# Optimization experiments

Hardware: AMD Instinct MI355X
Metric: run time of the kernel (lower is better)

The kernel has to match this reference:

```python
import jax, jax.numpy as jnp
import numpy as np

EPS = 1e-12

def l2_normalize(x, axis=-1):
    # matches torch F.normalize(p=2, dim=1, eps=1e-12) for 2D input
    n = jnp.sqrt(jnp.sum(x * x, axis=axis, keepdims=True))
    return x / jnp.maximum(n, EPS)

def setup_inputs() -> dict:
    key = jax.random.key(0)
    ks = jax.random.split(key, 7)
    N, D = 8192, 256
    s = 1.0 / np.sqrt(D)
    x = jax.random.normal(ks[0], (N, D), dtype=jnp.float32)
    Wq = jax.random.uniform(ks[1], (D, D), jnp.float32, -s, s)
    bq = jax.random.uniform(ks[2], (D,), jnp.float32, -s, s)
    Wk = jax.random.uniform(ks[3], (D, D), jnp.float32, -s, s)
    bk = jax.random.uniform(ks[4], (D,), jnp.float32, -s, s)
    Wv = jax.random.uniform(ks[5], (D, D), jnp.float32, -s, s)
    bv = jax.random.uniform(ks[6], (D,), jnp.float32, -s, s)
    return {"x": x, "Wq": Wq, "bq": bq, "Wk": Wk, "bk": bk, "Wv": Wv, "bv": bv}

def reference(x, Wq, bq, Wk, bk, Wv, bv):
    q = l2_normalize(x @ Wq.T + bq)           # [N, D]
    k = l2_normalize(x @ Wk.T + bk)           # [N, D]
    v = x @ Wv.T + bv                         # [N, D]
    cos_sim = q @ k.T                         # [N, N]
    w = jax.nn.relu(cos_sim)
    # zero diagonal, then renormalize rows to sum 1
    N = w.shape[0]
    w = jnp.where(jnp.eye(N, dtype=bool), 0.0, w)
    w = w / jnp.maximum(jnp.sum(w, axis=-1, keepdims=True), EPS)
    return w @ v + x
```

## Files before the change

### kernel.cpp

```cpp
#include <hip/hip_runtime.h>

#define NROWS 8192
#define DDIM  256
#define KSPLIT 4
#define BM 128
#define BK 64
#define NT (NROWS / KSPLIT / BK)

typedef __bf16 bf16x8 __attribute__((ext_vector_type(8)));
typedef float  f32x4  __attribute__((ext_vector_type(4)));
typedef float  f32x16 __attribute__((ext_vector_type(16)));

typedef __attribute__((address_space(1))) unsigned int uint_gas;
typedef __attribute__((address_space(3))) unsigned int uint_las;

__device__ __forceinline__ void gload_lds16(const void* g, void* l) {
  __builtin_amdgcn_global_load_lds((const uint_gas*)g, (uint_las*)l, 16, 0, 0);
}

__device__ __forceinline__ unsigned int f2bf_bits(float f) {
  union { float f; unsigned int u; } v; v.f = f;
  unsigned int r = v.u + 0x7FFFu + ((v.u >> 16) & 1u);
  return r >> 16;
}
__device__ __forceinline__ float bf2f(unsigned int b) {
  union { unsigned int u; float f; } v; v.u = b << 16;
  return v.f;
}
__device__ __forceinline__ unsigned int pack2bf(float a, float b) {
  union { unsigned int u; __bf16 h[2]; } p;
  p.h[0] = (__bf16)a; p.h[1] = (__bf16)b;
  return p.u;
}
__device__ __forceinline__ unsigned short f2h_bits(float f) {
  union { _Float16 h; unsigned short u; } c; c.h = (_Float16)f;
  return c.u;
}
__device__ __forceinline__ float h2f(unsigned short u) {
  union { unsigned short u; _Float16 h; } c; c.u = u;
  return (float)c.h;
}
__device__ __forceinline__ bf16x8 cvt8(const float* p) {
  float4 f0 = *(const float4*)p;
  float4 f1 = *(const float4*)(p + 4);
  union { bf16x8 v; unsigned short s[8]; } u;
  u.s[0] = (unsigned short)f2bf_bits(f0.x);
  u.s[1] = (unsigned short)f2bf_bits(f0.y);
  u.s[2] = (unsigned short)f2bf_bits(f0.z);
  u.s[3] = (unsigned short)f2bf_bits(f0.w);
  u.s[4] = (unsigned short)f2bf_bits(f1.x);
  u.s[5] = (unsigned short)f2bf_bits(f1.y);
  u.s[6] = (unsigned short)f2bf_bits(f1.z);
  u.s[7] = (unsigned short)f2bf_bits(f1.w);
  return u.v;
}

#define NWFRAG (3 * 16 * 8 * 64)
__global__ __launch_bounds__(256) void convert_kernel(
    const float* __restrict__ wq, const float* __restrict__ wk,
    const float* __restrict__ wv, unsigned short* __restrict__ Wp)
{
  int fid = blockIdx.x * 256 + threadIdx.x;
  if (fid >= NWFRAG) return;
  int l = fid & 63, ks = (fid >> 6) & 7, ct = (fid >> 9) & 15, out = fid >> 13;
  const float* src = (out == 0) ? wq : (out == 1) ? wk : wv;
  unsigned short* dst = Wp + (size_t)fid * 8;
  int row = ct * 16 + (l & 15), col = ks * 32 + (l >> 4) * 8;
  const float* p = src + (size_t)row * DDIM + col;
  float4 f0 = *(const float4*)p;
  float4 f1 = *(const float4*)(p + 4);
  ushort4 o0, o1;
  o0.x = (unsigned short)f2bf_bits(f0.x); o0.y = (unsigned short)f2bf_bits(f0.y);
  o0.z = (unsigned short)f2bf_bits(f0.z); o0.w = (unsigned short)f2bf_bits(f0.w);
  o1.x = (unsigned short)f2bf_bits(f1.x); o1.y = (unsigned short)f2bf_bits(f1.y);
  o1.z = (unsigned short)f2bf_bits(f1.z); o1.w = (unsigned short)f2bf_bits(f1.w);
  *(ushort4*)dst = o0;
  *(ushort4*)(dst + 4) = o1;
}

__global__ __launch_bounds__(256) void qkv_kernel(
    const float* __restrict__ bq, const float* __restrict__ bk, const float* __restrict__ bv,
    const float* __restrict__ x, const unsigned short* __restrict__ Wp,
    unsigned short* __restrict__ qb, unsigned short* __restrict__ kb,
    unsigned short* __restrict__ vtp)
{
  __shared__ unsigned short vstage[DDIM * 72];
  const int t = threadIdx.x;
  const int w = t >> 6, l = t & 63;
  const int c = l & 15, g = l >> 4;
  const int out = blockIdx.x / 128;
  const int mb  = blockIdx.x % 128;
  const int row0 = mb * 64;
  const int rw = row0 + w * 16;

  bf16x8 a[8];
  #pragma unroll
  for (int ks = 0; ks < 8; ks++)
    a[ks] = cvt8(x + (size_t)(rw + c) * DDIM + ks * 32 + g * 8);

  const float* bias = (out == 0) ? bq : (out == 1) ? bk : bv;
  f32x4 vals[16];
  #pragma unroll
  for (int ct = 0; ct < 16; ct++) {
    f32x4 acc = {0.f, 0.f, 0.f, 0.f};
    #pragma unroll
    for (int ks = 0; ks < 8; ks++) {
      bf16x8 b = *(const bf16x8*)(Wp + ((size_t)((out * 16 + ct) * 8 + ks) * 64 + l) * 8);
      acc = __builtin_amdgcn_mfma_f32_16x16x32_bf16(a[ks], b, acc, 0, 0, 0);
    }
    float bias_v = bias[ct * 16 + c];
    #pragma unroll
    for (int r = 0; r < 4; r++) acc[r] += bias_v;
    vals[ct] = acc;
  }
  if (out < 2) {
    #pragma unroll
    for (int r = 0; r < 4; r++) {
      float ss = 0.f;
      #pragma unroll
      for (int ct = 0; ct < 16; ct++) ss += vals[ct][r] * vals[ct][r];
      ss += __shfl_xor(ss, 1); ss += __shfl_xor(ss, 2);
      ss += __shfl_xor(ss, 4); ss += __shfl_xor(ss, 8);
      float inv = 1.f / fmaxf(sqrtf(ss), 1e-12f);
      #pragma unroll
      for (int ct = 0; ct < 16; ct++) vals[ct][r] *= inv;
    }
    unsigned short* dst = (out == 0) ? qb : kb;
    #pragma unroll
    for (int ct = 0; ct < 16; ct++) {
      #pragma unroll
      for (int r = 0; r < 4; r++) {
        unsigned int bits = f2bf_bits(vals[ct][r]);
        unsigned int ob = (unsigned int)__shfl_xor((int)bits, 1);
        if (!(l & 1))
          *(unsigned int*)(dst + (size_t)(rw + g * 4 + r) * DDIM + ct * 16 + c) =
              bits | (ob << 16);
      }
    }
  } else {
    #pragma unroll
    for (int ct = 0; ct < 16; ct++)
      #pragma unroll
      for (int r = 0; r < 4; r++)
        vstage[(ct * 16 + c) * 72 + (w * 16 + g * 4 + r)] =
            (unsigned short)f2bf_bits(vals[ct][r]);
    __syncthreads();
    unsigned short* wdst = vtp + (size_t)mb * 16384;
    #pragma unroll
    for (int p = 0; p < 8; p++) {
      int n = p * 256 + t;
      int dg = ((n >> 8) << 5) + (n & 31);
      int s  = (n >> 5) & 7;
      *(uint4*)(wdst + (size_t)n * 8) = *(const uint4*)(vstage + dg * 72 + s * 8);
    }
  }
}

__global__ __launch_bounds__(1024, 4) void attn_kernel(
    const unsigned short* __restrict__ qb, const unsigned short* __restrict__ kb,
    const unsigned short* __restrict__ vtp,
    unsigned short* __restrict__ nump, float* __restrict__ denp)
{
  __shared__ __align__(16) char smem[98304];
  char* kbuf = smem;
  char* Pb   = smem + 65536;

  const int t = threadIdx.x;
  const int w = t >> 6, l = t & 63;
  const int l31 = l & 31, hi = l >> 5;
  const int rw = w & 7;
  const int ts = t & 511;
  const int bid = blockIdx.x;
  const int split = bid & (KSPLIT - 1);
  const int mb = bid >> 2;
  const int q0 = mb * BM;
  const int kbase0 = split * (NROWS / KSPLIT);
  const char* kbc = (const char*)kb;
  const char* vtc = (const char*)vtp;

  if (w < 8) {
    const int sr = rw >> 1, sc = rw & 1;
    const int qrow = sr * 32 + l31;
    const int qrowg = q0 + qrow;
    const int krl = sc * 32 + l31;

    bf16x8 qa[16];
    {
      const unsigned short* qrowp = qb + (size_t)(q0 + qrow) * DDIM + hi * 8;
      #pragma unroll
      for (int m = 0; m < 16; m++) qa[m] = *(const bf16x8*)(qrowp + m * 16);
    }
    float denl = 0.f;

    auto stageK = [&](int buf, int it) {
      const char* ksrc = kbc + (size_t)(kbase0 + it * BK) * 512;
      #pragma unroll
      for (int i = 0; i < 4; i++) {
        int n = i * 512 + ts;
        int row = n >> 5, slot = n & 31;
        gload_lds16(ksrc + row * 512 + (((slot - row) & 31) << 4),
                    kbuf + buf * 32768 + i * 8192 + rw * 1024);
      }
    };

    stageK(0, 0);
    asm volatile("s_waitcnt vmcnt(0)" ::: "memory");
    __builtin_amdgcn_sched_barrier(0);
    __builtin_amdgcn_s_barrier();
    __builtin_amdgcn_sched_barrier(0);

    for (int it = 0; it < NT; ++it) {
      const int cur = it & 1;
      if (it + 1 < NT) stageK(cur ^ 1, it + 1);
      __builtin_amdgcn_sched_barrier(0);

      const char* kcur = kbuf + cur * 32768;
      f32x16 sacc = (f32x16){0.f};
      #pragma unroll
      for (int m = 0; m < 16; m++) {
        bf16x8 kf = *(const bf16x8*)(kcur + krl * 512 +
                                     (((m * 2 + hi + krl) & 31) << 4));
        sacc = __builtin_amdgcn_mfma_f32_32x32x16_bf16(kf, qa[m], sacc, 0, 0, 0);
      }
      char* pbase = Pb + cur * 16384 + sr * 4096 + l31 * 16 + hi * 8;
      const int kbase = kbase0 + it * BK;
      if (__builtin_expect(kbase < q0 + BM && q0 < kbase + BK, 0)) {
        const int dref = qrowg - (kbase + sc * 32 + hi * 4);
        #pragma unroll
        for (int q = 0; q < 4; q++) {
          float v0 = fmaxf(sacc[4 * q + 0], 0.f);
          float v1 = fmaxf(sacc[4 * q + 1], 0.f);
          float v2 = fmaxf(sacc[4 * q + 2], 0.f);
          float v3 = fmaxf(sacc[4 * q + 3], 0.f);
          const int d = dref - 8 * q;
          v0 = (d == 0) ? 0.f : v0;
          v1 = (d == 1) ? 0.f : v1;
          v2 = (d == 2) ? 0.f : v2;
          v3 = (d == 3) ? 0.f : v3;
          denl += (v0 + v1) + (v2 + v3);
          uint2 d2;
          d2.x = pack2bf(v0, v1);
          d2.y = pack2bf(v2, v3);
          *(uint2*)(pbase + (sc * 4 + q) * 512) = d2;
        }
      } else {
        #pragma unroll
        for (int q = 0; q < 4; q++) {
          float v0 = fmaxf(sacc[4 * q + 0], 0.f);
          float v1 = fmaxf(sacc[4 * q + 1], 0.f);
          float v2 = fmaxf(sacc[4 * q + 2], 0.f);
          float v3 = fmaxf(sacc[4 * q + 3], 0.f);
          denl += (v0 + v1) + (v2 + v3);
          uint2 d2;
          d2.x = pack2bf(v0, v1);
          d2.y = pack2bf(v2, v3);
          *(uint2*)(pbase + (sc * 4 + q) * 512) = d2;
        }
      }
      asm volatile("s_waitcnt vmcnt(0) lgkmcnt(0)" ::: "memory");
      __builtin_amdgcn_sched_barrier(0);
      __builtin_amdgcn_s_barrier();
      __builtin_amdgcn_sched_barrier(0);
    }

    float d = denl;
    d += __shfl_xor(d, 32);
    if (l < 32)
      denp[((size_t)split * 2 + sc) * NROWS + q0 + sr * 32 + l] = d;
  } else {
    const int pr = rw >> 2, pc = rw & 3;

    f32x16 oacc[2][2];
    #pragma unroll
    for (int rt = 0; rt < 2; rt++)
      #pragma unroll
      for (int dt = 0; dt < 2; dt++)
        oacc[rt][dt] = (f32x16){0.f};

    bf16x8 vfrA[8], vfrB[8];

    auto loadV = [&](bf16x8 (&dst)[8], int it) {
      const char* vsrc = vtc + (size_t)((kbase0 + it * BK) >> 6) * 32768;
      #pragma unroll
      for (int ch = 0; ch < 4; ch++)
        #pragma unroll
        for (int dt = 0; dt < 2; dt++)
          dst[ch * 2 + dt] = *(const bf16x8*)(vsrc + (pc * 2 + dt) * 4096 +
                                              (ch * 2 + hi) * 512 + l31 * 16);
    };
    auto pvcomp = [&](const bf16x8 (&vfr)[8], const char* Pprev) {
      #pragma unroll
      for (int ch = 0; ch < 4; ch++) {
        const int s512 = (ch * 2 + hi) * 512 + l31 * 16;
        bf16x8 pa0 = *(const bf16x8*)(Pprev + (pr * 2 + 0) * 4096 + s512);
        bf16x8 pa1 = *(const bf16x8*)(Pprev + (pr * 2 + 1) * 4096 + s512);
        #pragma unroll
        for (int dt = 0; dt < 2; dt++) {
          oacc[0][dt] = __builtin_amdgcn_mfma_f32_32x32x16_bf16(pa0, vfr[ch * 2 + dt],
                                                                oacc[0][dt], 0, 0, 0);
          oacc[1][dt] = __builtin_amdgcn_mfma_f32_32x32x16_bf16(pa1, vfr[ch * 2 + dt],
                                                                oacc[1][dt], 0, 0, 0);
        }
      }
    };

    __builtin_amdgcn_s_barrier();
    __builtin_amdgcn_sched_barrier(0);

    for (int it2 = 0; it2 < NT; it2 += 2) {
      loadV(vfrA, it2);
      if (it2 > 0) pvcomp(vfrB, Pb + 16384);
      asm volatile("s_waitcnt lgkmcnt(0)" ::: "memory");
      __builtin_amdgcn_sched_barrier(0);
      __builtin_amdgcn_s_barrier();
      __builtin_amdgcn_sched_barrier(0);
      loadV(vfrB, it2 + 1);
      pvcomp(vfrA, Pb + 0);
      asm volatile("s_waitcnt lgkmcnt(0)" ::: "memory");
      __builtin_amdgcn_sched_barrier(0);
      __builtin_amdgcn_s_barrier();
      __builtin_amdgcn_sched_barrier(0);
    }
    pvcomp(vfrB, Pb + 16384);

    unsigned short* np = nump + (size_t)split * NROWS * DDIM;
    #pragma unroll
    for (int rt = 0; rt < 2; rt++)
      #pragma unroll
      for (int dt = 0; dt < 2; dt++)
        #pragma unroll
        for (int r = 0; r < 16; r++) {
          int rowg = q0 + pr * 64 + rt * 32 + (r & 3) + 8 * (r >> 2) + 4 * hi;
          int col  = pc * 64 + dt * 32 + l31;
          np[(size_t)rowg * DDIM + col] = f2h_bits(oacc[rt][dt][r]);
        }
  }
}

__global__ __launch_bounds__(256) void combine_kernel(
    const float* __restrict__ x,
    const unsigned short* __restrict__ nump, const float* __restrict__ denp,
    float* __restrict__ out)
{
  const int t = threadIdx.x;
  const int w = t >> 6, l = t & 63;
  const int i = blockIdx.x * 4 + w;

  float den = 0.f;
  #pragma unroll
  for (int sp = 0; sp < KSPLIT * 2; sp++)
    den += denp[(size_t)sp * NROWS + i];
  float inv = 1.f / fmaxf(den, 1e-12f);

  const int d0 = l * 4;
  float4 acc = {0.f, 0.f, 0.f, 0.f};
  #pragma unroll
  for (int sp = 0; sp < KSPLIT; sp++) {
    ushort4 u4 = *(const ushort4*)(nump + ((size_t)sp * NROWS + i) * DDIM + d0);
    acc.x += h2f(u4.x); acc.y += h2f(u4.y);
    acc.z += h2f(u4.z); acc.w += h2f(u4.w);
  }
  float4 xx = *(const float4*)(x + (size_t)i * DDIM + d0);
  float4 o;
  o.x = acc.x * inv + xx.x;
  o.y = acc.y * inv + xx.y;
  o.z = acc.z * inv + xx.z;
  o.w = acc.w * inv + xx.w;
  *(float4*)(out + (size_t)i * DDIM + d0) = o;
}

extern "C" void kernel_launch(void* const* d_in, const int* in_sizes, int n_in,
                              void* d_out, int out_size, void* d_ws, size_t ws_size,
                              hipStream_t stream)
{
  const float* x  = (const float*)d_in[0];
  const float* Wq = (const float*)d_in[1];
  const float* bq = (const float*)d_in[2];
  const float* Wk = (const float*)d_in[3];
  const float* bk = (const float*)d_in[4];
  const float* Wv = (const float*)d_in[5];
  const float* bv = (const float*)d_in[6];

  char* ws = (char*)d_ws;
  unsigned short* Wp   = (unsigned short*)(ws + 0);
  unsigned short* qb   = (unsigned short*)(ws + 393216);
  unsigned short* kb   = (unsigned short*)(ws + 4587520);
  unsigned short* vtp  = (unsigned short*)(ws + 8781824);
  unsigned short* nump = (unsigned short*)(ws + 12976128);
  float* denp = (float*)(ws + 29753344);

  convert_kernel<<<96, 256, 0, stream>>>(Wq, Wk, Wv, Wp);
  qkv_kernel<<<384, 256, 0, stream>>>(bq, bk, bv, x, Wp, qb, kb, vtp);
  attn_kernel<<<(NROWS / BM) * KSPLIT, 1024, 0, stream>>>(qb, kb, vtp, nump, denp);
  combine_kernel<<<NROWS / 4, 256, 0, stream>>>(x, nump, denp, (float*)d_out);
}
```

Measured before the change: 125.1 us.

## Fuse split-K combine into attention kernel via last-block atomic counter

Removes the separate combine kernel launch. Each attention block increments a per-row-block counter after a thread fence, and the last of the four split blocks sums the partial numerators and denominators, normalizes, adds the residual and writes the output. This saves a kernel launch and its tail, but adds fences, an atomic and a serialized combine tail in the last-finishing block. The counters are zeroed in the convert kernel.

```diff
diff --git a/kernel.cpp b/kernel.cpp
--- a/kernel.cpp
+++ b/kernel.cpp
@@ -58,8 +58,10 @@
 #define NWFRAG (3 * 16 * 8 * 64)
 __global__ __launch_bounds__(256) void convert_kernel(
     const float* __restrict__ wq, const float* __restrict__ wk,
-    const float* __restrict__ wv, unsigned short* __restrict__ Wp)
+    const float* __restrict__ wv, unsigned short* __restrict__ Wp,
+    int* __restrict__ fincnt)
 {
+  if (blockIdx.x == 0 && threadIdx.x < 128) fincnt[threadIdx.x] = 0;
   int fid = blockIdx.x * 256 + threadIdx.x;
   if (fid >= NWFRAG) return;
   int l = fid & 63, ks = (fid >> 6) & 7, ct = (fid >> 9) & 15, out = fid >> 13;
@@ -159,9 +161,13 @@
 __global__ __launch_bounds__(1024, 4) void attn_kernel(
     const unsigned short* __restrict__ qb, const unsigned short* __restrict__ kb,
     const unsigned short* __restrict__ vtp,
-    unsigned short* __restrict__ nump, float* __restrict__ denp)
+    unsigned short* __restrict__ nump, float* __restrict__ denp,
+    const float* __restrict__ x, float* __restrict__ outp,
+    int* __restrict__ fincnt)
 {
   __shared__ __align__(16) char smem[98304];
+  __shared__ float invr[128];
+  __shared__ int done_sh;
   char* kbuf = smem;
   char* Pb   = smem + 65536;
 
@@ -335,38 +341,43 @@
           np[(size_t)rowg * DDIM + col] = f2h_bits(oacc[rt][dt][r]);
         }
   }
-}
-
-__global__ __launch_bounds__(256) void combine_kernel(
-    const float* __restrict__ x,
-    const unsigned short* __restrict__ nump, const float* __restrict__ denp,
-    float* __restrict__ out)
-{
-  const int t = threadIdx.x;
-  const int w = t >> 6, l = t & 63;
-  const int i = blockIdx.x * 4 + w;
-
-  float den = 0.f;
-  #pragma unroll
-  for (int sp = 0; sp < KSPLIT * 2; sp++)
-    den += denp[(size_t)sp * NROWS + i];
-  float inv = 1.f / fmaxf(den, 1e-12f);
-
-  const int d0 = l * 4;
-  float4 acc = {0.f, 0.f, 0.f, 0.f};
-  #pragma unroll
-  for (int sp = 0; sp < KSPLIT; sp++) {
-    ushort4 u4 = *(const ushort4*)(nump + ((size_t)sp * NROWS + i) * DDIM + d0);
-    acc.x += h2f(u4.x); acc.y += h2f(u4.y);
-    acc.z += h2f(u4.z); acc.w += h2f(u4.w);
+
+  __syncthreads();
+  __threadfence();
+  __syncthreads();
+  if (t == 0) done_sh = atomicAdd(fincnt + mb, 1);
+  __syncthreads();
+  if (done_sh == 3) {
+    __threadfence();
+    if (t < 128) {
+      float den = 0.f;
+      #pragma unroll
+      for (int s = 0; s < 8; s++) den += denp[(size_t)s * NROWS + q0 + t];
+      invr[t] = 1.f / fmaxf(den, 1e-12f);
+    }
+    __syncthreads();
+    #pragma unroll
+    for (int i = 0; i < 8; i++) {
+      int id = i * 1024 + t;
+      int row = id >> 6, c4 = id & 63;
+      int rowg = q0 + row;
+      float inv = invr[row];
+      float4 acc = {0.f, 0.f, 0.f, 0.f};
+      #pragma unroll
+      for (int sp = 0; sp < KSPLIT; sp++) {
+        ushort4 u4 = *(const ushort4*)(nump + ((size_t)sp * NROWS + rowg) * DDIM + c4 * 4);
+        acc.x += h2f(u4.x); acc.y += h2f(u4.y);
+        acc.z += h2f(u4.z); acc.w += h2f(u4.w);
+      }
+      float4 xx = *(const float4*)(x + (size_t)rowg * DDIM + c4 * 4);
+      float4 o;
+      o.x = acc.x * inv + xx.x;
+      o.y = acc.y * inv + xx.y;
+      o.z = acc.z * inv + xx.z;
+      o.w = acc.w * inv + xx.w;
+      *(float4*)(outp + (size_t)rowg * DDIM + c4 * 4) = o;
+    }
   }
-  float4 xx = *(const float4*)(x + (size_t)i * DDIM + d0);
-  float4 o;
-  o.x = acc.x * inv + xx.x;
-  o.y = acc.y * inv + xx.y;
-  o.z = acc.z * inv + xx.z;
-  o.w = acc.w * inv + xx.w;
-  *(float4*)(out + (size_t)i * DDIM + d0) = o;
 }
 
 extern "C" void kernel_launch(void* const* d_in, const int* in_sizes, int n_in,
@@ -388,9 +399,10 @@
   unsigned short* vtp  = (unsigned short*)(ws + 8781824);
   unsigned short* nump = (unsigned short*)(ws + 12976128);
   float* denp = (float*)(ws + 29753344);
-
-  convert_kernel<<<96, 256, 0, stream>>>(Wq, Wk, Wv, Wp);
+  int* fincnt = (int*)(ws + 30015488);
+
+  convert_kernel<<<96, 256, 0, stream>>>(Wq, Wk, Wv, Wp, fincnt);
   qkv_kernel<<<384, 256, 0, stream>>>(bq, bk, bv, x, Wp, qb, kb, vtp);
-  attn_kernel<<<(NROWS / BM) * KSPLIT, 1024, 0, stream>>>(qb, kb, vtp, nump, denp);
-  combine_kernel<<<NROWS / 4, 256, 0, stream>>>(x, nump, denp, (float*)d_out);
-}
+  attn_kernel<<<(NROWS / BM) * KSPLIT, 1024, 0, stream>>>(qb, kb, vtp, nump, denp,
+                                                          x, (float*)d_out, fincnt);
+}
```

New measurement: 243.0 us. 94.2% more time.
